# Performance work log

Hardware: AMD Instinct MI355X
Metric: run time of the kernel (lower is better)

## Reference

```python
import jax
import jax.numpy as jnp
from jax import lax
import numpy as np

N_BITS = 24
OUT_BITS = 48
BATCH = 131072

# Shift tensor: S[i, j, i+j] = 1, used to place partial product i (24 bits)
# into a 48-bit lane shifted left by i (LSB-first layout).
_ii, _jj = np.meshgrid(np.arange(N_BITS), np.arange(N_BITS), indexing='ij')
_S = np.zeros((N_BITS, N_BITS, OUT_BITS), dtype=np.float32)
_S[_ii, _jj, _ii + _jj] = 1.0
SHIFT = jnp.asarray(_S)


def bit_add(a, b):
    """Ripple-carry binary adder on LSB-first bit vectors.
    a, b: [..., 48] with entries in {0,1}. Returns sum bits [..., 48]
    (carry out of bit 47 is discarded; 24x24 product never overflows 48 bits)."""
    a_t = jnp.moveaxis(a, -1, 0)  # [48, ...]
    b_t = jnp.moveaxis(b, -1, 0)

    def step(carry, ab):
        ai, bi = ab
        t = ai + bi + carry          # 0..3
        s = jnp.mod(t, 2.0)          # sum bit (XOR of three inputs)
        c = jnp.floor(t * 0.5)       # majority carry
        return c, s

    c0 = jnp.zeros(a_t.shape[1:], dtype=a.dtype)
    _, s = lax.scan(step, c0, (a_t, b_t))
    return jnp.moveaxis(s, 0, -1)


def reference(A, B):
    """A, B: [..., 24] LSB-first bits -> product bits [..., 48] LSB-first."""
    # Partial products: pp[i, j] = B_i AND A_j (AND == product for {0,1} spikes)
    M = B[..., :, None] * A[..., None, :]                 # [..., 24(i), 24(j)]
    # Zero-pad/shift each row i left by i bits into 48-bit lanes
    pp = jnp.einsum('...ij,ijk->...ik', M, SHIFT)         # [..., 24, 48]
    pps = jnp.moveaxis(pp, -2, 0)                         # [24, ..., 48]

    # Parallel (tree) accumulation, O(log n) adder levels: 24->12->6->3->2->1
    while pps.shape[0] > 1:
        n = pps.shape[0]
        even = pps[: (n // 2) * 2]
        summed = bit_add(even[0::2], even[1::2])
        if n % 2 == 1:
            summed = jnp.concatenate([summed, pps[-1:]], axis=0)
        pps = summed
    return pps[0]


def setup_inputs() -> dict:
    key = jax.random.key(0)
    kA, kB = jax.random.split(key)
    A = jax.random.randint(kA, (BATCH, N_BITS), 0, 2).astype(jnp.float32)
    B = jax.random.randint(kB, (BATCH, N_BITS), 0, 2).astype(jnp.float32)
    return {"A": A, "B": B}
```

## Files before the change

kernel.cpp:

```cpp
#include <hip/hip_runtime.h>
#include <stdint.h>


#define NBATCH 131072
#define RPB    256
#define NF4IN  (RPB * 6)

__global__ __launch_bounds__(256) void ArrayMultiplier24x24_kernel(
    const uint4* __restrict__ A4,
    const uint4* __restrict__ B4,
    float4* __restrict__ O4)
{
    __shared__ uint32_t nibA[NF4IN];
    __shared__ uint32_t nibB[NF4IN];
    __shared__ uint32_t packA[RPB];
    __shared__ uint32_t packB[RPB];

    const int t = threadIdx.x;
    const size_t inBase  = (size_t)blockIdx.x * NF4IN;
    const size_t outBase = (size_t)blockIdx.x * (RPB * 12);

#pragma unroll
    for (int k = 0; k < 6; ++k) {
        int f = k * 256 + t;
        uint4 va = A4[inBase + f];
        uint4 vb = B4[inBase + f];
        uint32_t na = ((va.x >> 29) & 1u) | ((va.y >> 28) & 2u) |
                      ((va.z >> 27) & 4u) | ((va.w >> 26) & 8u);
        uint32_t nb = ((vb.x >> 29) & 1u) | ((vb.y >> 28) & 2u) |
                      ((vb.z >> 27) & 4u) | ((vb.w >> 26) & 8u);
        nibA[f] = na;
        nibB[f] = nb;
    }
    __syncthreads();

    uint32_t a = 0u, b = 0u;
#pragma unroll
    for (int s = 0; s < 6; ++s) {
        a |= nibA[t * 6 + s] << (4 * s);
        b |= nibB[t * 6 + s] << (4 * s);
    }
    packA[t] = a;
    packB[t] = b;
    __syncthreads();

#pragma unroll
    for (int k = 0; k < 12; ++k) {
        int g = k * 256 + t;
        int row = g / 12;
        int c0 = (g - row * 12) * 4;
        uint64_t p = (uint64_t)packA[row] * (uint64_t)packB[row];
        float4 v;
        v.x = (float)((uint32_t)(p >> (c0 + 0)) & 1u);
        v.y = (float)((uint32_t)(p >> (c0 + 1)) & 1u);
        v.z = (float)((uint32_t)(p >> (c0 + 2)) & 1u);
        v.w = (float)((uint32_t)(p >> (c0 + 3)) & 1u);
        O4[outBase + g] = v;
    }
}

extern "C" void kernel_launch(void* const* d_in, const int* in_sizes, int n_in,
                              void* d_out, int out_size, void* d_ws, size_t ws_size,
                              hipStream_t stream)
{
    const uint4* A4 = (const uint4*)d_in[0];
    const uint4* B4 = (const uint4*)d_in[1];
    float4* O4 = (float4*)d_out;

    const int blocks = NBATCH / RPB;
    ArrayMultiplier24x24_kernel<<<blocks, 256, 0, stream>>>(A4, B4, O4);
}
```

Before: 76.66 us.

## Replace shared-memory staging and block barriers with per-wave shuffles

Each 64-lane wave now handles 32 rows on its own. Nibble packing and product distribution move from LDS plus __syncthreads to cross-lane __shfl, which removes block-level synchronisation and shared-memory traffic. Each row's product is computed once per row rather than once per output float4. The cost is many more shuffle instructions, redundant shuffles with selects, and half the lanes idle during the multiply. The kernel is memory-bound, so the gain may be limited.

```diff
diff --git a/kernel.cpp b/kernel.cpp
--- a/kernel.cpp
+++ b/kernel.cpp
@@ -3,58 +3,68 @@
 
 
 #define NBATCH 131072
-#define RPB    256
-#define NF4IN  (RPB * 6)
+#define ROWS_PER_WAVE 32
+#define N_WAVES (NBATCH / ROWS_PER_WAVE)
+#define WAVES_PER_BLOCK 4
+#define N_BLOCKS (N_WAVES / WAVES_PER_BLOCK)
 
 __global__ __launch_bounds__(256) void ArrayMultiplier24x24_kernel(
     const uint4* __restrict__ A4,
     const uint4* __restrict__ B4,
     float4* __restrict__ O4)
 {
-    __shared__ uint32_t nibA[NF4IN];
-    __shared__ uint32_t nibB[NF4IN];
-    __shared__ uint32_t packA[RPB];
-    __shared__ uint32_t packB[RPB];
+    const int l = threadIdx.x & 63;
+    const int w = blockIdx.x * WAVES_PER_BLOCK + (threadIdx.x >> 6);
+    const size_t inBase  = (size_t)w * (ROWS_PER_WAVE * 6);
+    const size_t outBase = (size_t)w * (ROWS_PER_WAVE * 12);
 
-    const int t = threadIdx.x;
-    const size_t inBase  = (size_t)blockIdx.x * NF4IN;
-    const size_t outBase = (size_t)blockIdx.x * (RPB * 12);
+    uint32_t nA[3], nB[3];
+#pragma unroll
+    for (int k = 0; k < 3; ++k) {
+        uint4 va = A4[inBase + k * 64 + l];
+        uint4 vb = B4[inBase + k * 64 + l];
+        nA[k] = ((va.x >> 29) & 1u) | ((va.y >> 28) & 2u) |
+                ((va.z >> 27) & 4u) | ((va.w >> 26) & 8u);
+        nB[k] = ((vb.x >> 29) & 1u) | ((vb.y >> 28) & 2u) |
+                ((vb.z >> 27) & 4u) | ((vb.w >> 26) & 8u);
+    }
+
+    const int r = l & 31;
+    uint32_t a = 0u, b = 0u;
+#pragma unroll
+    for (int s = 0; s < 6; ++s) {
+        int idx = r * 6 + s;
+        int src = idx & 63;
+        int k   = idx >> 6;
+        uint32_t a0 = __shfl(nA[0], src, 64);
+        uint32_t a1 = __shfl(nA[1], src, 64);
+        uint32_t a2 = __shfl(nA[2], src, 64);
+        uint32_t b0 = __shfl(nB[0], src, 64);
+        uint32_t b1 = __shfl(nB[1], src, 64);
+        uint32_t b2 = __shfl(nB[2], src, 64);
+        uint32_t av = (k == 0) ? a0 : ((k == 1) ? a1 : a2);
+        uint32_t bv = (k == 0) ? b0 : ((k == 1) ? b1 : b2);
+        a |= av << (4 * s);
+        b |= bv << (4 * s);
+    }
+
+    uint64_t p = (uint64_t)a * (uint64_t)b;
+    uint32_t plo = (uint32_t)p, phi = (uint32_t)(p >> 32);
 
 #pragma unroll
     for (int k = 0; k < 6; ++k) {
-        int f = k * 256 + t;
-        uint4 va = A4[inBase + f];
-        uint4 vb = B4[inBase + f];
-        uint32_t na = ((va.x >> 29) & 1u) | ((va.y >> 28) & 2u) |
-                      ((va.z >> 27) & 4u) | ((va.w >> 26) & 8u);
-        uint32_t nb = ((vb.x >> 29) & 1u) | ((vb.y >> 28) & 2u) |
-                      ((vb.z >> 27) & 4u) | ((vb.w >> 26) & 8u);
-        nibA[f] = na;
-        nibB[f] = nb;
-    }
-    __syncthreads();
-
-    uint32_t a = 0u, b = 0u;
-#pragma unroll
-    for (int s = 0; s < 6; ++s) {
-        a |= nibA[t * 6 + s] << (4 * s);
-        b |= nibB[t * 6 + s] << (4 * s);
-    }
-    packA[t] = a;
-    packB[t] = b;
-    __syncthreads();
-
-#pragma unroll
-    for (int k = 0; k < 12; ++k) {
-        int g = k * 256 + t;
+        int g = k * 64 + l;
         int row = g / 12;
         int c0 = (g - row * 12) * 4;
-        uint64_t p = (uint64_t)packA[row] * (uint64_t)packB[row];
+        uint32_t lo = __shfl(plo, row, 64);
+        uint32_t hi = __shfl(phi, row, 64);
+        uint64_t pp = ((uint64_t)hi << 32) | lo;
+        uint32_t bits = (uint32_t)(pp >> c0);
         float4 v;
-        v.x = (float)((uint32_t)(p >> (c0 + 0)) & 1u);
-        v.y = (float)((uint32_t)(p >> (c0 + 1)) & 1u);
-        v.z = (float)((uint32_t)(p >> (c0 + 2)) & 1u);
-        v.w = (float)((uint32_t)(p >> (c0 + 3)) & 1u);
+        v.x = (float)(bits & 1u);
+        v.y = (float)((bits >> 1) & 1u);
+        v.z = (float)((bits >> 2) & 1u);
+        v.w = (float)((bits >> 3) & 1u);
         O4[outBase + g] = v;
     }
 }
@@ -67,6 +77,5 @@
     const uint4* B4 = (const uint4*)d_in[1];
     float4* O4 = (float4*)d_out;
 
-    const int blocks = NBATCH / RPB;
-    ArrayMultiplier24x24_kernel<<<blocks, 256, 0, stream>>>(A4, B4, O4);
+    ArrayMultiplier24x24_kernel<<<N_BLOCKS, 256, 0, stream>>>(A4, B4, O4);
 }
```

After: 76.21 us (median of 2 runs). No clear change (-0.6%).
